# Optimization experiments

Measured on AMD Instinct MI355X. Metric: run time of the kernel, lower is better.

Reference implementation:

```python
import jax, jax.numpy as jnp
import numpy as np

N_NODES = 100000
N_EDGES = 1600000
NUM_RELS = 200
NUM_BASES = 4
IN_FEAT = 20   # hardcoded by `view(-1, 1, 20)` in the torch source
OUT_FEAT = 20
SUBMAT_IN = IN_FEAT // NUM_BASES   # 5
SUBMAT_OUT = OUT_FEAT // NUM_BASES # 5


def setup_inputs() -> dict:
    key = jax.random.key(0)
    ks = jax.random.split(key, 9)
    return {
        "h": jax.random.normal(ks[0], (N_NODES, IN_FEAT), dtype=jnp.float32),
        "weight": jax.random.normal(ks[1], (NUM_RELS, NUM_BASES * SUBMAT_IN * SUBMAT_OUT), dtype=jnp.float32),
        "bias_term": jax.random.normal(ks[2], (NUM_RELS, OUT_FEAT), dtype=jnp.float32),
        "gate_weight": jax.random.normal(ks[3], (NUM_RELS, OUT_FEAT, 1), dtype=jnp.float32),
        "gate_bias": jax.random.normal(ks[4], (NUM_RELS, 1), dtype=jnp.float32),
        "loop_weight": jax.random.normal(ks[5], (IN_FEAT, OUT_FEAT), dtype=jnp.float32),
        "edge_src": jax.random.randint(ks[6], (N_EDGES,), 0, N_NODES, dtype=jnp.int32),
        "edge_dst": jax.random.randint(ks[7], (N_EDGES,), 0, N_NODES, dtype=jnp.int32),
        "etype": jax.random.randint(ks[8], (NUM_RELS,), 0, NUM_RELS, dtype=jnp.int32) if False else jax.random.randint(ks[8], (N_EDGES,), 0, NUM_RELS, dtype=jnp.int32),
    }


def reference(h, weight, bias_term, gate_weight, gate_bias, loop_weight, edge_src, edge_dst, etype):
    n_nodes = h.shape[0]
    # self-loop message (dropout=0.0 -> identity)
    loop_message = h @ loop_weight                                    # [N, out]
    # per-edge relation-indexed gathers
    W = weight[etype].reshape(-1, NUM_BASES, SUBMAT_IN, SUBMAT_OUT)   # [E, B, si, so]
    src = h[edge_src]                                                 # [E, in]
    node = src.reshape(-1, NUM_BASES, SUBMAT_IN)                      # [E, B, si]
    # block-diagonal small matmul
    msg = jnp.einsum('ebi,ebio->ebo', node, W).reshape(-1, OUT_FEAT)  # [E, out]
    # gate: sigmoid(<full src node, gate_weight_r> + gate_bias_r)
    gw = gate_weight[etype, :, 0]                                     # [E, out(=20=in)]
    gb = gate_bias[etype, 0]                                          # [E]
    gate = jax.nn.sigmoid(jnp.sum(src * gw, axis=-1) + gb)            # [E]
    msg = gate[:, None] * (msg + bias_term[etype])                    # [E, out]
    # scatter-sum aggregation to destination nodes (zero init for isolated nodes)
    agg = jax.ops.segment_sum(msg, edge_dst, num_segments=n_nodes)    # [N, out]
    return jax.nn.relu(agg + loop_message)
```

## Files before the change

kernel.cpp:

```cpp
#include <hip/hip_runtime.h>
#include <hip/hip_fp16.h>
#include <math.h>

#define IN_FEAT 20
#define OUT_FEAT 20
#define NUM_BASES 4
#define SUBMAT_IN 5
#define SUBMAT_OUT 5
#define NUM_RELS 200
#define CAP 64
#define NPB 160
#define BCAP 3072

__global__ void zero_kernel(int* __restrict__ p, int n) {
    int i = blockIdx.x * blockDim.x + threadIdx.x;
    if (i < n) p[i] = 0;
}

__global__ void __launch_bounds__(1024)
bucket_scatter_kernel(const int* __restrict__ edge_src,
                      const int* __restrict__ edge_dst,
                      const int* __restrict__ etype,
                      int* __restrict__ cursor,
                      int2* __restrict__ bucketed,
                      int n_edges, int nb) {
    __shared__ int lhist[1024];
    __shared__ int lbase[1024];
    __shared__ int lrank[1024];
    int tid = threadIdx.x;
    for (int i = tid; i < nb; i += 1024) { lhist[i] = 0; lrank[i] = 0; }
    __syncthreads();

    int e0 = blockIdx.x * 4096 + tid * 4;
    int s[4], d[4], t[4], bk[4];
    bool val[4];
    if (e0 + 3 < n_edges) {
        int4 sv = *(const int4*)(edge_src + e0);
        int4 dv = *(const int4*)(edge_dst + e0);
        int4 tv = *(const int4*)(etype + e0);
        s[0]=sv.x; s[1]=sv.y; s[2]=sv.z; s[3]=sv.w;
        d[0]=dv.x; d[1]=dv.y; d[2]=dv.z; d[3]=dv.w;
        t[0]=tv.x; t[1]=tv.y; t[2]=tv.z; t[3]=tv.w;
        val[0]=val[1]=val[2]=val[3]=true;
    } else {
#pragma unroll
        for (int k = 0; k < 4; ++k) {
            int e = e0 + k;
            val[k] = (e < n_edges);
            s[k] = val[k] ? edge_src[e] : 0;
            d[k] = val[k] ? edge_dst[e] : 0;
            t[k] = val[k] ? etype[e] : 0;
        }
    }
#pragma unroll
    for (int k = 0; k < 4; ++k) {
        bk[k] = d[k] / NPB;
        if (val[k]) atomicAdd(&lhist[bk[k]], 1);
    }
    __syncthreads();
    for (int i = tid; i < nb; i += 1024)
        if (lhist[i] > 0) lbase[i] = atomicAdd(&cursor[i], lhist[i]);
    __syncthreads();
#pragma unroll
    for (int k = 0; k < 4; ++k) {
        if (val[k]) {
            int r = atomicAdd(&lrank[bk[k]], 1);
            int off = lbase[bk[k]] + r;
            if (off < BCAP) {
                unsigned packed = (unsigned)s[k] | ((unsigned)t[k] << 17);
                bucketed[(size_t)bk[k] * BCAP + off] = make_int2(d[k], (int)packed);
            }
        }
    }
}

__global__ void __launch_bounds__(1024)
bucket_place_kernel(const int* __restrict__ cursor,
                    const int2* __restrict__ bucketed,
                    unsigned* __restrict__ records,
                    int* __restrict__ cnt,
                    int n_nodes) {
    __shared__ unsigned img[NPB * CAP];
    __shared__ int lcnt[NPB];
    int b = blockIdx.x, tid = threadIdx.x;
    int node0 = b * NPB;
    for (int i = tid; i < NPB; i += 1024) lcnt[i] = 0;
    __syncthreads();
    int m = cursor[b]; if (m > BCAP) m = BCAP;
    for (int i = tid; i < m; i += 1024) {
        int2 r = bucketed[(size_t)b * BCAP + i];
        int dl = r.x - node0;
        int sl = atomicAdd(&lcnt[dl], 1);
        if (sl < CAP) img[dl * CAP + sl] = (unsigned)r.y;
    }
    __syncthreads();
    for (int i = tid; i < NPB; i += 1024) {
        int v = node0 + i;
        if (v < n_nodes) cnt[v] = lcnt[i];
    }
    const int W4 = NPB * CAP / 4;
    uint4* g4 = (uint4*)records + (size_t)node0 * (CAP / 4);
    const uint4* l4 = (const uint4*)img;
    for (int i = tid; i < W4; i += 1024) {
        int v = node0 + (i / (CAP / 4));
        if (v < n_nodes) g4[i] = l4[i];
    }
}

__global__ void __launch_bounds__(1024, 4)
gather_kernel(const float* __restrict__ h,
              const float* __restrict__ loop_weight,
              const float* __restrict__ weight,
              const float* __restrict__ bias_term,
              const float* __restrict__ gate_weight,
              const float* __restrict__ gate_bias,
              const int* __restrict__ cnt,
              const unsigned* __restrict__ records,
              float* __restrict__ out, int n_nodes, int n_groups) {
    __shared__ __half lds_wt[100 * NUM_RELS];
    __shared__ float  lds_gwt[IN_FEAT * NUM_RELS];
    __shared__ float  lds_gb[NUM_RELS];
    __shared__ float  lds_lw[IN_FEAT * OUT_FEAT];
    int tid = threadIdx.x;
    for (int idx = tid; idx < 100 * NUM_RELS; idx += 1024) {
        int t = idx / 100, j = idx % 100;
        lds_wt[j * NUM_RELS + t] = __float2half(weight[idx]);
    }
    for (int idx = tid; idx < IN_FEAT * NUM_RELS; idx += 1024) {
        int t = idx / IN_FEAT, i = idx % IN_FEAT;
        lds_gwt[i * NUM_RELS + t] = gate_weight[idx];
    }
    for (int idx = tid; idx < NUM_RELS; idx += 1024) lds_gb[idx] = gate_bias[idx];
    for (int idx = tid; idx < IN_FEAT * OUT_FEAT; idx += 1024) lds_lw[idx] = loop_weight[idx];
    __syncthreads();

    int wave = blockIdx.x * 16 + (tid >> 6);
    int nwaves = gridDim.x * 16;
    int l = tid & 63;
    int l16 = l & 15;

    for (int grp = wave; grp < n_groups; grp += nwaves) {
        int v = grp * 4 + (l >> 4);
        bool valid = (v < n_nodes);
        int c = valid ? cnt[v] : 0;
        if (c > CAP) c = CAP;

        float acc[OUT_FEAT];
#pragma unroll
        for (int j = 0; j < OUT_FEAT; ++j) acc[j] = 0.0f;

        if (valid) {
#pragma unroll
            for (int i0 = 0; i0 < 2; ++i0) {
                int i = l16 + i0 * 16;
                if (i < IN_FEAT) {
                    float s = h[(size_t)v * IN_FEAT + i];
#pragma unroll
                    for (int j = 0; j < OUT_FEAT; ++j)
                        acc[j] = fmaf(s, lds_lw[i * OUT_FEAT + j], acc[j]);
                }
            }
        }

#pragma unroll
        for (int it = 0; it < 4; ++it) {
            int slot = l16 + it * 16;
            if (valid && slot < c) {
                unsigned p = records[(size_t)v * CAP + slot];
                int srcid = (int)(p & 0x1FFFFu);
                int t = (int)(p >> 17);

                float src[IN_FEAT];
                const float4* hp = (const float4*)(h + (size_t)srcid * IN_FEAT);
#pragma unroll
                for (int i = 0; i < IN_FEAT / 4; ++i) {
                    float4 tv = hp[i];
                    src[4 * i + 0] = tv.x; src[4 * i + 1] = tv.y;
                    src[4 * i + 2] = tv.z; src[4 * i + 3] = tv.w;
                }

                float g = lds_gb[t];
#pragma unroll
                for (int i = 0; i < IN_FEAT; ++i)
                    g = fmaf(src[i], lds_gwt[i * NUM_RELS + t], g);
                g = 1.0f / (1.0f + __expf(-g));

                const __half* wt = lds_wt + t;
#pragma unroll
                for (int b = 0; b < NUM_BASES; ++b) {
#pragma unroll
                    for (int i = 0; i < SUBMAT_IN; ++i) {
                        float sv = g * src[b * SUBMAT_IN + i];
#pragma unroll
                        for (int o = 0; o < SUBMAT_OUT; ++o) {
                            float w = __half2float(wt[(size_t)(b * 25 + i * 5 + o) * NUM_RELS]);
                            acc[b * SUBMAT_OUT + o] = fmaf(sv, w, acc[b * SUBMAT_OUT + o]);
                        }
                    }
                }
                const float4* btp = (const float4*)(bias_term + (size_t)t * OUT_FEAT);
#pragma unroll
                for (int k = 0; k < OUT_FEAT / 4; ++k) {
                    float4 bv = btp[k];
                    acc[4 * k + 0] = fmaf(g, bv.x, acc[4 * k + 0]);
                    acc[4 * k + 1] = fmaf(g, bv.y, acc[4 * k + 1]);
                    acc[4 * k + 2] = fmaf(g, bv.z, acc[4 * k + 2]);
                    acc[4 * k + 3] = fmaf(g, bv.w, acc[4 * k + 3]);
                }
            }
        }

#pragma unroll
        for (int mask = 8; mask > 0; mask >>= 1) {
#pragma unroll
            for (int j = 0; j < OUT_FEAT; ++j)
                acc[j] += __shfl_xor(acc[j], mask, 16);
        }

        if (valid && l16 < OUT_FEAT / 4) {
            float4 tv;
            tv.x = fmaxf(acc[4 * l16 + 0], 0.0f);
            tv.y = fmaxf(acc[4 * l16 + 1], 0.0f);
            tv.z = fmaxf(acc[4 * l16 + 2], 0.0f);
            tv.w = fmaxf(acc[4 * l16 + 3], 0.0f);
            ((float4*)(out + (size_t)v * OUT_FEAT))[l16] = tv;
        }
    }
}

__global__ void loop_msg_kernel(const float* __restrict__ h,
                                const float* __restrict__ loop_weight,
                                float* __restrict__ out, int n_nodes) {
    int v = blockIdx.x * blockDim.x + threadIdx.x;
    if (v >= n_nodes) return;
    float src[IN_FEAT];
    const float4* hp = (const float4*)(h + (size_t)v * IN_FEAT);
#pragma unroll
    for (int i = 0; i < IN_FEAT / 4; ++i) {
        float4 t = hp[i];
        src[4 * i + 0] = t.x; src[4 * i + 1] = t.y;
        src[4 * i + 2] = t.z; src[4 * i + 3] = t.w;
    }
    float acc[OUT_FEAT];
#pragma unroll
    for (int j = 0; j < OUT_FEAT; ++j) acc[j] = 0.0f;
#pragma unroll
    for (int i = 0; i < IN_FEAT; ++i) {
        float s = src[i];
#pragma unroll
        for (int j = 0; j < OUT_FEAT; ++j)
            acc[j] = fmaf(s, loop_weight[i * OUT_FEAT + j], acc[j]);
    }
    float4* op = (float4*)(out + (size_t)v * OUT_FEAT);
#pragma unroll
    for (int j = 0; j < OUT_FEAT / 4; ++j) {
        float4 t;
        t.x = acc[4 * j + 0]; t.y = acc[4 * j + 1];
        t.z = acc[4 * j + 2]; t.w = acc[4 * j + 3];
        op[j] = t;
    }
}

__global__ void edge_atomic_kernel(const float* __restrict__ h,
                                   const float* __restrict__ weight,
                                   const float* __restrict__ bias_term,
                                   const float* __restrict__ gate_weight,
                                   const float* __restrict__ gate_bias,
                                   const int* __restrict__ edge_src,
                                   const int* __restrict__ edge_dst,
                                   const int* __restrict__ etype,
                                   float* __restrict__ out, int n_edges) {
    int e = blockIdx.x * blockDim.x + threadIdx.x;
    if (e >= n_edges) return;
    int s = edge_src[e], d = edge_dst[e], t = etype[e];
    float src[IN_FEAT];
    const float4* hp = (const float4*)(h + (size_t)s * IN_FEAT);
#pragma unroll
    for (int i = 0; i < IN_FEAT / 4; ++i) {
        float4 v = hp[i];
        src[4 * i + 0] = v.x; src[4 * i + 1] = v.y;
        src[4 * i + 2] = v.z; src[4 * i + 3] = v.w;
    }
    const float* W = weight + (size_t)t * 100;
    float msg[OUT_FEAT];
#pragma unroll
    for (int j = 0; j < OUT_FEAT; ++j) msg[j] = 0.0f;
#pragma unroll
    for (int b = 0; b < NUM_BASES; ++b)
#pragma unroll
        for (int i = 0; i < SUBMAT_IN; ++i) {
            float sv = src[b * SUBMAT_IN + i];
#pragma unroll
            for (int o = 0; o < SUBMAT_OUT; ++o)
                msg[b * SUBMAT_OUT + o] =
                    fmaf(sv, W[(b * SUBMAT_IN + i) * SUBMAT_OUT + o],
                         msg[b * SUBMAT_OUT + o]);
        }
    const float* gw = gate_weight + (size_t)t * OUT_FEAT;
    float g = gate_bias[t];
#pragma unroll
    for (int i = 0; i < IN_FEAT; ++i) g = fmaf(src[i], gw[i], g);
    g = 1.0f / (1.0f + __expf(-g));
    const float* bt = bias_term + (size_t)t * OUT_FEAT;
    float* dstp = out + (size_t)d * OUT_FEAT;
#pragma unroll
    for (int j = 0; j < OUT_FEAT; ++j) atomicAdd(&dstp[j], g * (msg[j] + bt[j]));
}

__global__ void relu_kernel(float* __restrict__ out, int n4) {
    int i = blockIdx.x * blockDim.x + threadIdx.x;
    if (i >= n4) return;
    float4* p = (float4*)out;
    float4 v = p[i];
    v.x = fmaxf(v.x, 0.0f); v.y = fmaxf(v.y, 0.0f);
    v.z = fmaxf(v.z, 0.0f); v.w = fmaxf(v.w, 0.0f);
    p[i] = v;
}

extern "C" void kernel_launch(void* const* d_in, const int* in_sizes, int n_in,
                              void* d_out, int out_size, void* d_ws, size_t ws_size,
                              hipStream_t stream) {
    const float* h           = (const float*)d_in[0];
    const float* weight      = (const float*)d_in[1];
    const float* bias_term   = (const float*)d_in[2];
    const float* gate_weight = (const float*)d_in[3];
    const float* gate_bias   = (const float*)d_in[4];
    const float* loop_weight = (const float*)d_in[5];
    const int* edge_src      = (const int*)d_in[6];
    const int* edge_dst      = (const int*)d_in[7];
    const int* etype         = (const int*)d_in[8];
    float* out = (float*)d_out;

    const int n_nodes = in_sizes[0] / IN_FEAT;
    const int n_edges = in_sizes[6];
    const int nb = (n_nodes + NPB - 1) / NPB;

    size_t off_cursor   = 0;
    size_t off_bucketed = (((size_t)nb * 4 + 127) / 128) * 128;
    size_t off_records  = ((off_bucketed + (size_t)nb * BCAP * 8 + 127) / 128) * 128;
    size_t off_cnt      = ((off_records + (size_t)n_nodes * CAP * 4 + 127) / 128) * 128;
    size_t need = off_cnt + (size_t)n_nodes * 4;

    bool ok = (ws_size >= need) && (n_nodes <= (1 << 17)) && (nb <= 1024) &&
              (in_sizes[4] == NUM_RELS) && (in_sizes[1] == NUM_RELS * 100) &&
              (in_sizes[5] == IN_FEAT * OUT_FEAT);

    if (ok) {
        int*  cursor   = (int*)((char*)d_ws + off_cursor);
        int2* bucketed = (int2*)((char*)d_ws + off_bucketed);
        unsigned* records = (unsigned*)((char*)d_ws + off_records);
        int*  cnt      = (int*)((char*)d_ws + off_cnt);

        zero_kernel<<<(nb + 255) / 256, 256, 0, stream>>>(cursor, nb);
        bucket_scatter_kernel<<<(n_edges + 4095) / 4096, 1024, 0, stream>>>(
            edge_src, edge_dst, etype, cursor, bucketed, n_edges, nb);
        bucket_place_kernel<<<nb, 1024, 0, stream>>>(
            cursor, bucketed, records, cnt, n_nodes);
        int n_groups = (n_nodes + 3) / 4;
        gather_kernel<<<512, 1024, 0, stream>>>(
            h, loop_weight, weight, bias_term, gate_weight, gate_bias,
            cnt, records, out, n_nodes, n_groups);
    } else {
        loop_msg_kernel<<<(n_nodes + 255) / 256, 256, 0, stream>>>(
            h, loop_weight, out, n_nodes);
        edge_atomic_kernel<<<(n_edges + 255) / 256, 256, 0, stream>>>(
            h, weight, bias_term, gate_weight, gate_bias,
            edge_src, edge_dst, etype, out, n_edges);
        relu_kernel<<<(n_nodes * OUT_FEAT / 4 + 255) / 256, 256, 0, stream>>>(
            out, n_nodes * OUT_FEAT / 4);
    }
}
```

Baseline: 205.7 us.

## Replace two-pass bucket sort with direct per-node atomic scatter and repack weights

```diff
diff --git a/kernel.cpp b/kernel.cpp
--- a/kernel.cpp
+++ b/kernel.cpp
@@ -9,30 +9,21 @@
 #define SUBMAT_OUT 5
 #define NUM_RELS 200
 #define CAP 64
-#define NPB 160
-#define BCAP 3072
 
 __global__ void zero_kernel(int* __restrict__ p, int n) {
     int i = blockIdx.x * blockDim.x + threadIdx.x;
     if (i < n) p[i] = 0;
 }
 
-__global__ void __launch_bounds__(1024)
-bucket_scatter_kernel(const int* __restrict__ edge_src,
-                      const int* __restrict__ edge_dst,
-                      const int* __restrict__ etype,
-                      int* __restrict__ cursor,
-                      int2* __restrict__ bucketed,
-                      int n_edges, int nb) {
-    __shared__ int lhist[1024];
-    __shared__ int lbase[1024];
-    __shared__ int lrank[1024];
-    int tid = threadIdx.x;
-    for (int i = tid; i < nb; i += 1024) { lhist[i] = 0; lrank[i] = 0; }
-    __syncthreads();
-
-    int e0 = blockIdx.x * 4096 + tid * 4;
-    int s[4], d[4], t[4], bk[4];
+__global__ void __launch_bounds__(256)
+scatter_kernel(const int* __restrict__ edge_src,
+               const int* __restrict__ edge_dst,
+               const int* __restrict__ etype,
+               int* __restrict__ cnt,
+               unsigned* __restrict__ records,
+               int n_edges) {
+    int e0 = (blockIdx.x * 256 + threadIdx.x) * 4;
+    int s[4], d[4], t[4];
     bool val[4];
     if (e0 + 3 < n_edges) {
         int4 sv = *(const int4*)(edge_src + e0);
@@ -54,60 +45,17 @@
     }
 #pragma unroll
     for (int k = 0; k < 4; ++k) {
-        bk[k] = d[k] / NPB;
-        if (val[k]) atomicAdd(&lhist[bk[k]], 1);
-    }
-    __syncthreads();
-    for (int i = tid; i < nb; i += 1024)
-        if (lhist[i] > 0) lbase[i] = atomicAdd(&cursor[i], lhist[i]);
-    __syncthreads();
-#pragma unroll
-    for (int k = 0; k < 4; ++k) {
         if (val[k]) {
-            int r = atomicAdd(&lrank[bk[k]], 1);
-            int off = lbase[bk[k]] + r;
-            if (off < BCAP) {
+            int slot = atomicAdd(&cnt[d[k]], 1);
+            if (slot < CAP) {
                 unsigned packed = (unsigned)s[k] | ((unsigned)t[k] << 17);
-                bucketed[(size_t)bk[k] * BCAP + off] = make_int2(d[k], (int)packed);
+                records[(size_t)d[k] * CAP + slot] = packed;
             }
         }
     }
 }
 
-__global__ void __launch_bounds__(1024)
-bucket_place_kernel(const int* __restrict__ cursor,
-                    const int2* __restrict__ bucketed,
-                    unsigned* __restrict__ records,
-                    int* __restrict__ cnt,
-                    int n_nodes) {
-    __shared__ unsigned img[NPB * CAP];
-    __shared__ int lcnt[NPB];
-    int b = blockIdx.x, tid = threadIdx.x;
-    int node0 = b * NPB;
-    for (int i = tid; i < NPB; i += 1024) lcnt[i] = 0;
-    __syncthreads();
-    int m = cursor[b]; if (m > BCAP) m = BCAP;
-    for (int i = tid; i < m; i += 1024) {
-        int2 r = bucketed[(size_t)b * BCAP + i];
-        int dl = r.x - node0;
-        int sl = atomicAdd(&lcnt[dl], 1);
-        if (sl < CAP) img[dl * CAP + sl] = (unsigned)r.y;
-    }
-    __syncthreads();
-    for (int i = tid; i < NPB; i += 1024) {
-        int v = node0 + i;
-        if (v < n_nodes) cnt[v] = lcnt[i];
-    }
-    const int W4 = NPB * CAP / 4;
-    uint4* g4 = (uint4*)records + (size_t)node0 * (CAP / 4);
-    const uint4* l4 = (const uint4*)img;
-    for (int i = tid; i < W4; i += 1024) {
-        int v = node0 + (i / (CAP / 4));
-        if (v < n_nodes) g4[i] = l4[i];
-    }
-}
-
-__global__ void __launch_bounds__(1024, 4)
+__global__ void __launch_bounds__(1024, 8)
 gather_kernel(const float* __restrict__ h,
               const float* __restrict__ loop_weight,
               const float* __restrict__ weight,
@@ -117,17 +65,18 @@
               const int* __restrict__ cnt,
               const unsigned* __restrict__ records,
               float* __restrict__ out, int n_nodes, int n_groups) {
-    __shared__ __half lds_wt[100 * NUM_RELS];
-    __shared__ float  lds_gwt[IN_FEAT * NUM_RELS];
-    __shared__ float  lds_gb[NUM_RELS];
-    __shared__ float  lds_lw[IN_FEAT * OUT_FEAT];
+    __shared__ __half2 lds_wp[NUM_RELS * 51];
+    __shared__ float   lds_gwt[IN_FEAT * NUM_RELS];
+    __shared__ float   lds_gb[NUM_RELS];
+    __shared__ float   lds_lw[IN_FEAT * OUT_FEAT];
     int tid = threadIdx.x;
-    for (int idx = tid; idx < 100 * NUM_RELS; idx += 1024) {
-        int t = idx / 100, j = idx % 100;
-        lds_wt[j * NUM_RELS + t] = __float2half(weight[idx]);
+    for (int idx = tid; idx < NUM_RELS * 50; idx += 1024) {
+        int t = idx / 50, f = idx - t * 50;
+        lds_wp[t * 51 + f] = __floats2half2_rn(weight[t * 100 + f],
+                                               weight[t * 100 + f + 50]);
     }
     for (int idx = tid; idx < IN_FEAT * NUM_RELS; idx += 1024) {
-        int t = idx / IN_FEAT, i = idx % IN_FEAT;
+        int t = idx / IN_FEAT, i = idx - t * IN_FEAT;
         lds_gwt[i * NUM_RELS + t] = gate_weight[idx];
     }
     for (int idx = tid; idx < NUM_RELS; idx += 1024) lds_gb[idx] = gate_bias[idx];
@@ -185,19 +134,21 @@
                     g = fmaf(src[i], lds_gwt[i * NUM_RELS + t], g);
                 g = 1.0f / (1.0f + __expf(-g));
 
-                const __half* wt = lds_wt + t;
-#pragma unroll
-                for (int b = 0; b < NUM_BASES; ++b) {
-#pragma unroll
-                    for (int i = 0; i < SUBMAT_IN; ++i) {
-                        float sv = g * src[b * SUBMAT_IN + i];
-#pragma unroll
-                        for (int o = 0; o < SUBMAT_OUT; ++o) {
-                            float w = __half2float(wt[(size_t)(b * 25 + i * 5 + o) * NUM_RELS]);
-                            acc[b * SUBMAT_OUT + o] = fmaf(sv, w, acc[b * SUBMAT_OUT + o]);
-                        }
-                    }
+#pragma unroll
+                for (int i = 0; i < IN_FEAT; ++i) src[i] *= g;
+
+                const __half2* wp = lds_wp + t * 51;
+#pragma unroll
+                for (int f = 0; f < 50; ++f) {
+                    float2 w = __half22float2(wp[f]);
+                    const int b0 = f / 25, r = f - b0 * 25;
+                    const int i0 = r / 5, o0 = r - i0 * 5;
+                    acc[b0 * 5 + o0] =
+                        fmaf(src[b0 * 5 + i0], w.x, acc[b0 * 5 + o0]);
+                    acc[(b0 + 2) * 5 + o0] =
+                        fmaf(src[(b0 + 2) * 5 + i0], w.y, acc[(b0 + 2) * 5 + o0]);
                 }
+
                 const float4* btp = (const float4*)(bias_term + (size_t)t * OUT_FEAT);
 #pragma unroll
                 for (int k = 0; k < OUT_FEAT / 4; ++k) {
@@ -333,29 +284,22 @@
 
     const int n_nodes = in_sizes[0] / IN_FEAT;
     const int n_edges = in_sizes[6];
-    const int nb = (n_nodes + NPB - 1) / NPB;
-
-    size_t off_cursor   = 0;
-    size_t off_bucketed = (((size_t)nb * 4 + 127) / 128) * 128;
-    size_t off_records  = ((off_bucketed + (size_t)nb * BCAP * 8 + 127) / 128) * 128;
-    size_t off_cnt      = ((off_records + (size_t)n_nodes * CAP * 4 + 127) / 128) * 128;
+
+    size_t off_records = 0;
+    size_t off_cnt     = (((size_t)n_nodes * CAP * 4 + 127) / 128) * 128;
     size_t need = off_cnt + (size_t)n_nodes * 4;
 
-    bool ok = (ws_size >= need) && (n_nodes <= (1 << 17)) && (nb <= 1024) &&
+    bool ok = (ws_size >= need) && (n_nodes <= (1 << 17)) &&
               (in_sizes[4] == NUM_RELS) && (in_sizes[1] == NUM_RELS * 100) &&
               (in_sizes[5] == IN_FEAT * OUT_FEAT);
 
     if (ok) {
-        int*  cursor   = (int*)((char*)d_ws + off_cursor);
-        int2* bucketed = (int2*)((char*)d_ws + off_bucketed);
         unsigned* records = (unsigned*)((char*)d_ws + off_records);
         int*  cnt      = (int*)((char*)d_ws + off_cnt);
 
-        zero_kernel<<<(nb + 255) / 256, 256, 0, stream>>>(cursor, nb);
-        bucket_scatter_kernel<<<(n_edges + 4095) / 4096, 1024, 0, stream>>>(
-            edge_src, edge_dst, etype, cursor, bucketed, n_edges, nb);
-        bucket_place_kernel<<<nb, 1024, 0, stream>>>(
-            cursor, bucketed, records, cnt, n_nodes);
+        zero_kernel<<<(n_nodes + 255) / 256, 256, 0, stream>>>(cnt, n_nodes);
+        scatter_kernel<<<(n_edges + 1023) / 1024, 256, 0, stream>>>(
+            edge_src, edge_dst, etype, cnt, records, n_edges);
         int n_groups = (n_nodes + 3) / 4;
         gather_kernel<<<512, 1024, 0, stream>>>(
             h, loop_weight, weight, bias_term, gate_weight, gate_bias,
```

Result: slower. 556.2 us (+170.4%).

## Switch to compact CSR records, fp16 padded node features, and paired-weight LDS layout

Applied to the files above, without the earlier changes.

```diff
diff --git a/kernel.cpp b/kernel.cpp
--- a/kernel.cpp
+++ b/kernel.cpp
@@ -11,6 +11,7 @@
 #define CAP 64
 #define NPB 160
 #define BCAP 3072
+
 
 __global__ void zero_kernel(int* __restrict__ p, int n) {
     int i = blockIdx.x * blockDim.x + threadIdx.x;
@@ -75,59 +76,113 @@
 }
 
 __global__ void __launch_bounds__(1024)
-bucket_place_kernel(const int* __restrict__ cursor,
-                    const int2* __restrict__ bucketed,
-                    unsigned* __restrict__ records,
-                    int* __restrict__ cnt,
-                    int n_nodes) {
-    __shared__ unsigned img[NPB * CAP];
+bucket_scan_kernel(const int* __restrict__ cursor, int* __restrict__ bucket_base,
+                   int nb) {
+    __shared__ int s[1024];
+    int tid = threadIdx.x;
+    int v = (tid < nb) ? min(cursor[tid], BCAP) : 0;
+    s[tid] = v;
+    __syncthreads();
+    for (int step = 1; step < 1024; step <<= 1) {
+        int t = (tid >= step) ? s[tid - step] : 0;
+        __syncthreads();
+        if (tid >= step) s[tid] += t;
+        __syncthreads();
+    }
+    if (tid < nb) bucket_base[tid] = s[tid] - v;
+}
+
+__global__ void __launch_bounds__(1024)
+place_csr_kernel(const int* __restrict__ cursor,
+                 const int* __restrict__ bucket_base,
+                 const int2* __restrict__ bucketed,
+                 unsigned* __restrict__ records,
+                 int* __restrict__ cnt,
+                 int* __restrict__ off,
+                 int n_nodes) {
     __shared__ int lcnt[NPB];
+    __shared__ int sscan[NPB];
+    __shared__ int lrank[NPB];
     int b = blockIdx.x, tid = threadIdx.x;
     int node0 = b * NPB;
-    for (int i = tid; i < NPB; i += 1024) lcnt[i] = 0;
+    if (tid < NPB) { lcnt[tid] = 0; lrank[tid] = 0; }
     __syncthreads();
     int m = cursor[b]; if (m > BCAP) m = BCAP;
+    int gbase = bucket_base[b];
+
+    for (int i = tid; i < m; i += 1024) {
+        int2 r = bucketed[(size_t)b * BCAP + i];
+        atomicAdd(&lcnt[r.x - node0], 1);
+    }
+    __syncthreads();
+    if (tid < NPB) sscan[tid] = lcnt[tid];
+    __syncthreads();
+    for (int step = 1; step < NPB; step <<= 1) {
+        int t = (tid < NPB && tid >= step) ? sscan[tid - step] : 0;
+        __syncthreads();
+        if (tid < NPB && tid >= step) sscan[tid] += t;
+        __syncthreads();
+    }
+    if (tid < NPB) {
+        int excl = sscan[tid] - lcnt[tid];
+        int v = node0 + tid;
+        if (v < n_nodes) { cnt[v] = lcnt[tid]; off[v] = gbase + excl; }
+        sscan[tid] = excl;
+    }
+    __syncthreads();
     for (int i = tid; i < m; i += 1024) {
         int2 r = bucketed[(size_t)b * BCAP + i];
         int dl = r.x - node0;
-        int sl = atomicAdd(&lcnt[dl], 1);
-        if (sl < CAP) img[dl * CAP + sl] = (unsigned)r.y;
-    }
-    __syncthreads();
-    for (int i = tid; i < NPB; i += 1024) {
-        int v = node0 + i;
-        if (v < n_nodes) cnt[v] = lcnt[i];
-    }
-    const int W4 = NPB * CAP / 4;
-    uint4* g4 = (uint4*)records + (size_t)node0 * (CAP / 4);
-    const uint4* l4 = (const uint4*)img;
-    for (int i = tid; i < W4; i += 1024) {
-        int v = node0 + (i / (CAP / 4));
-        if (v < n_nodes) g4[i] = l4[i];
-    }
+        int rk = atomicAdd(&lrank[dl], 1);
+        records[(size_t)gbase + sscan[dl] + rk] = (unsigned)r.y;
+    }
+}
+
+__global__ void __launch_bounds__(256)
+hpad_kernel(const float* __restrict__ h, __half* __restrict__ h_pad, int n_nodes) {
+    int v = blockIdx.x * 256 + threadIdx.x;
+    if (v >= n_nodes) return;
+    const float4* hp = (const float4*)(h + (size_t)v * IN_FEAT);
+    float4 a = hp[0], b = hp[1], c = hp[2], d = hp[3], e = hp[4];
+    __half2 p0 = __floats2half2_rn(a.x, a.y), p1 = __floats2half2_rn(a.z, a.w);
+    __half2 p2 = __floats2half2_rn(b.x, b.y), p3 = __floats2half2_rn(b.z, b.w);
+    __half2 p4 = __floats2half2_rn(c.x, c.y), p5 = __floats2half2_rn(c.z, c.w);
+    __half2 p6 = __floats2half2_rn(d.x, d.y), p7 = __floats2half2_rn(d.z, d.w);
+    __half2 p8 = __floats2half2_rn(e.x, e.y), p9 = __floats2half2_rn(e.z, e.w);
+    uint4 w0, w1; uint2 w2;
+    w0.x = *(unsigned*)&p0; w0.y = *(unsigned*)&p1; w0.z = *(unsigned*)&p2; w0.w = *(unsigned*)&p3;
+    w1.x = *(unsigned*)&p4; w1.y = *(unsigned*)&p5; w1.z = *(unsigned*)&p6; w1.w = *(unsigned*)&p7;
+    w2.x = *(unsigned*)&p8; w2.y = *(unsigned*)&p9;
+    char* dst = (char*)(h_pad + (size_t)v * 32);
+    *(uint4*)(dst)      = w0;
+    *(uint4*)(dst + 16) = w1;
+    *(uint2*)(dst + 32) = w2;
 }
 
 __global__ void __launch_bounds__(1024, 4)
 gather_kernel(const float* __restrict__ h,
+              const __half* __restrict__ h_pad,
               const float* __restrict__ loop_weight,
               const float* __restrict__ weight,
               const float* __restrict__ bias_term,
               const float* __restrict__ gate_weight,
               const float* __restrict__ gate_bias,
               const int* __restrict__ cnt,
+              const int* __restrict__ off,
               const unsigned* __restrict__ records,
               float* __restrict__ out, int n_nodes, int n_groups) {
-    __shared__ __half lds_wt[100 * NUM_RELS];
-    __shared__ float  lds_gwt[IN_FEAT * NUM_RELS];
-    __shared__ float  lds_gb[NUM_RELS];
-    __shared__ float  lds_lw[IN_FEAT * OUT_FEAT];
+    __shared__ __half2 lds_wp[NUM_RELS * 51];
+    __shared__ float   lds_gwt[IN_FEAT * NUM_RELS];
+    __shared__ float   lds_gb[NUM_RELS];
+    __shared__ float   lds_lw[IN_FEAT * OUT_FEAT];
     int tid = threadIdx.x;
-    for (int idx = tid; idx < 100 * NUM_RELS; idx += 1024) {
-        int t = idx / 100, j = idx % 100;
-        lds_wt[j * NUM_RELS + t] = __float2half(weight[idx]);
+    for (int idx = tid; idx < NUM_RELS * 50; idx += 1024) {
+        int t = idx / 50, f = idx - t * 50;
+        lds_wp[t * 51 + f] = __floats2half2_rn(weight[t * 100 + f],
+                                               weight[t * 100 + f + 50]);
     }
     for (int idx = tid; idx < IN_FEAT * NUM_RELS; idx += 1024) {
-        int t = idx / IN_FEAT, i = idx % IN_FEAT;
+        int t = idx / IN_FEAT, i = idx - t * IN_FEAT;
         lds_gwt[i * NUM_RELS + t] = gate_weight[idx];
     }
     for (int idx = tid; idx < NUM_RELS; idx += 1024) lds_gb[idx] = gate_bias[idx];
@@ -142,7 +197,8 @@
     for (int grp = wave; grp < n_groups; grp += nwaves) {
         int v = grp * 4 + (l >> 4);
         bool valid = (v < n_nodes);
-        int c = valid ? cnt[v] : 0;
+        int c = 0, base = 0;
+        if (valid) { c = cnt[v]; base = off[v]; }
         if (c > CAP) c = CAP;
 
         float acc[OUT_FEAT];
@@ -166,17 +222,23 @@
         for (int it = 0; it < 4; ++it) {
             int slot = l16 + it * 16;
             if (valid && slot < c) {
-                unsigned p = records[(size_t)v * CAP + slot];
+                unsigned p = records[(size_t)base + slot];
                 int srcid = (int)(p & 0x1FFFFu);
                 int t = (int)(p >> 17);
 
+                const char* sp = (const char*)(h_pad + (size_t)srcid * 32);
+                uint4 A = *(const uint4*)(sp);
+                uint4 B = *(const uint4*)(sp + 16);
+                uint2 C = *(const uint2*)(sp + 32);
                 float src[IN_FEAT];
-                const float4* hp = (const float4*)(h + (size_t)srcid * IN_FEAT);
-#pragma unroll
-                for (int i = 0; i < IN_FEAT / 4; ++i) {
-                    float4 tv = hp[i];
-                    src[4 * i + 0] = tv.x; src[4 * i + 1] = tv.y;
-                    src[4 * i + 2] = tv.z; src[4 * i + 3] = tv.w;
+                {
+                    unsigned u[10] = {A.x, A.y, A.z, A.w, B.x, B.y, B.z, B.w, C.x, C.y};
+#pragma unroll
+                    for (int q = 0; q < 10; ++q) {
+                        __half2 hv = *reinterpret_cast<__half2*>(&u[q]);
+                        float2 f = __half22float2(hv);
+                        src[2 * q] = f.x; src[2 * q + 1] = f.y;
+                    }
                 }
 
                 float g = lds_gb[t];
@@ -185,19 +247,21 @@
                     g = fmaf(src[i], lds_gwt[i * NUM_RELS + t], g);
                 g = 1.0f / (1.0f + __expf(-g));
 
-                const __half* wt = lds_wt + t;
-#pragma unroll
-                for (int b = 0; b < NUM_BASES; ++b) {
-#pragma unroll
-                    for (int i = 0; i < SUBMAT_IN; ++i) {
-                        float sv = g * src[b * SUBMAT_IN + i];
-#pragma unroll
-                        for (int o = 0; o < SUBMAT_OUT; ++o) {
-                            float w = __half2float(wt[(size_t)(b * 25 + i * 5 + o) * NUM_RELS]);
-                            acc[b * SUBMAT_OUT + o] = fmaf(sv, w, acc[b * SUBMAT_OUT + o]);
-                        }
-                    }
+#pragma unroll
+                for (int i = 0; i < IN_FEAT; ++i) src[i] *= g;
+
+                const __half2* wp = lds_wp + t * 51;
+#pragma unroll
+                for (int f = 0; f < 50; ++f) {
+                    float2 w = __half22float2(wp[f]);
+                    const int b0 = f / 25, r = f - b0 * 25;
+                    const int i0 = r / 5, o0 = r - i0 * 5;
+                    acc[b0 * 5 + o0] =
+                        fmaf(src[b0 * 5 + i0], w.x, acc[b0 * 5 + o0]);
+                    acc[(b0 + 2) * 5 + o0] =
+                        fmaf(src[(b0 + 2) * 5 + i0], w.y, acc[(b0 + 2) * 5 + o0]);
                 }
+
                 const float4* btp = (const float4*)(bias_term + (size_t)t * OUT_FEAT);
 #pragma unroll
                 for (int k = 0; k < OUT_FEAT / 4; ++k) {
@@ -336,30 +400,38 @@
     const int nb = (n_nodes + NPB - 1) / NPB;
 
     size_t off_cursor   = 0;
-    size_t off_bucketed = (((size_t)nb * 4 + 127) / 128) * 128;
+    size_t off_bbase    = (((size_t)nb * 4 + 127) / 128) * 128;
+    size_t off_bucketed = ((off_bbase + (size_t)nb * 4 + 127) / 128) * 128;
     size_t off_records  = ((off_bucketed + (size_t)nb * BCAP * 8 + 127) / 128) * 128;
-    size_t off_cnt      = ((off_records + (size_t)n_nodes * CAP * 4 + 127) / 128) * 128;
-    size_t need = off_cnt + (size_t)n_nodes * 4;
+    size_t off_cnt      = ((off_records + (size_t)n_edges * 4 + 127) / 128) * 128;
+    size_t off_offs     = ((off_cnt + (size_t)n_nodes * 4 + 127) / 128) * 128;
+    size_t off_hpad     = ((off_offs + (size_t)n_nodes * 4 + 127) / 128) * 128;
+    size_t need = off_hpad + (size_t)n_nodes * 64;
 
     bool ok = (ws_size >= need) && (n_nodes <= (1 << 17)) && (nb <= 1024) &&
               (in_sizes[4] == NUM_RELS) && (in_sizes[1] == NUM_RELS * 100) &&
               (in_sizes[5] == IN_FEAT * OUT_FEAT);
 
     if (ok) {
-        int*  cursor   = (int*)((char*)d_ws + off_cursor);
-        int2* bucketed = (int2*)((char*)d_ws + off_bucketed);
+        int*  cursor      = (int*)((char*)d_ws + off_cursor);
+        int*  bucket_base = (int*)((char*)d_ws + off_bbase);
+        int2* bucketed    = (int2*)((char*)d_ws + off_bucketed);
         unsigned* records = (unsigned*)((char*)d_ws + off_records);
-        int*  cnt      = (int*)((char*)d_ws + off_cnt);
+        int*  cnt         = (int*)((char*)d_ws + off_cnt);
+        int*  off         = (int*)((char*)d_ws + off_offs);
+        __half* h_pad     = (__half*)((char*)d_ws + off_hpad);
 
         zero_kernel<<<(nb + 255) / 256, 256, 0, stream>>>(cursor, nb);
+        hpad_kernel<<<(n_nodes + 255) / 256, 256, 0, stream>>>(h, h_pad, n_nodes);
         bucket_scatter_kernel<<<(n_edges + 4095) / 4096, 1024, 0, stream>>>(
             edge_src, edge_dst, etype, cursor, bucketed, n_edges, nb);
-        bucket_place_kernel<<<nb, 1024, 0, stream>>>(
-            cursor, bucketed, records, cnt, n_nodes);
+        bucket_scan_kernel<<<1, 1024, 0, stream>>>(cursor, bucket_base, nb);
+        place_csr_kernel<<<nb, 1024, 0, stream>>>(
+            cursor, bucket_base, bucketed, records, cnt, off, n_nodes);
         int n_groups = (n_nodes + 3) / 4;
         gather_kernel<<<512, 1024, 0, stream>>>(
-            h, loop_weight, weight, bias_term, gate_weight, gate_bias,
-            cnt, records, out, n_nodes, n_groups);
+            h, h_pad, loop_weight, weight, bias_term, gate_weight, gate_bias,
+            cnt, off, records, out, n_nodes, n_groups);
     } else {
         loop_msg_kernel<<<(n_nodes + 255) / 256, 256, 0, stream>>>(
             h, loop_weight, out, n_nodes);
```

New measurement: 205.9 us. Within noise of the previous version (+0.1%).
